# Optimization experiments

Measured on AMD Instinct MI355X. Metric: run time of the kernel, lower is better.

## Reference

```python
import jax, jax.numpy as jnp
import numpy as np

B, N, E, C = 8, 4096, 1024, 512


def setup_inputs() -> dict:
    key = jax.random.key(0)
    k1, k2, k3, k4 = jax.random.split(key, 4)
    node_feats = jax.random.normal(k1, (B, N, C), dtype=jnp.float32)
    hyper_feats = jax.random.normal(k2, (B, E, C), dtype=jnp.float32)
    # torch nn.Linear params: weight [out, in], bias [out]
    Wq = jax.random.normal(k3, (C, C), dtype=jnp.float32) * (1.0 / np.sqrt(C))
    bq = jnp.zeros((C,), dtype=jnp.float32)
    Wkv = jax.random.normal(k4, (2 * C, C), dtype=jnp.float32) * (1.0 / np.sqrt(C))
    bkv = jnp.zeros((2 * C,), dtype=jnp.float32)
    return {"node_feats": node_feats, "hyper_feats": hyper_feats,
            "Wq": Wq, "bq": bq, "Wkv": Wkv, "bkv": bkv}


def reference(node_feats, hyper_feats, Wq, bq, Wkv, bkv):
    C_ = node_feats.shape[-1]
    scale = C_ ** -0.5
    Q = node_feats @ Wq.T + bq                      # [B,N,C]
    KV = hyper_feats @ Wkv.T + bkv                  # [B,E,2C]
    K, V = KV[..., :C_], KV[..., C_:]               # [B,E,C] each
    attn = jnp.einsum('bnc,bec->bne', Q, K) * scale  # [B,N,E]
    attn = jax.nn.softmax(attn, axis=-1)
    return jnp.einsum('bne,bec->bnc', attn, V)       # [B,N,C]
```

## Files before the change

kernel.cpp:

```cpp
#include <hip/hip_runtime.h>
#include <cstdint>
#include <cstddef>

typedef _Float16 h16;
typedef _Float16 h16x4 __attribute__((ext_vector_type(4)));
typedef _Float16 h16x8 __attribute__((ext_vector_type(8)));
typedef float fx4 __attribute__((ext_vector_type(4)));

static constexpr int B_ = 8, N_ = 4096, E_ = 1024, C_ = 512;
static constexpr float SCALE = 0.044194173824159216f;

__device__ __forceinline__ void glds16(const h16* g, h16* l) {
  __builtin_amdgcn_global_load_lds(
      (const __attribute__((address_space(1))) unsigned int*)g,
      (__attribute__((address_space(3))) unsigned int*)l, 16, 0, 0);
}

__global__ __launch_bounds__(256) void cvt_kernel(const float* __restrict__ src,
                                                  h16* __restrict__ dst, int n8) {
  int i = blockIdx.x * 256 + threadIdx.x;
  if (i >= n8) return;
  const float4* s4 = (const float4*)src;
  float4 a = s4[2 * i], b = s4[2 * i + 1];
  h16x8 o;
  o[0] = (h16)a.x; o[1] = (h16)a.y; o[2] = (h16)a.z; o[3] = (h16)a.w;
  o[4] = (h16)b.x; o[5] = (h16)b.y; o[6] = (h16)b.z; o[7] = (h16)b.w;
  *(h16x8*)(dst + (size_t)i * 8) = o;
}

template <int MODE>
__global__ __launch_bounds__(256) void gemm_bt(
    const void* __restrict__ Ap, const h16* __restrict__ Bm,
    const float* __restrict__ bias,
    h16* __restrict__ outH, h16* __restrict__ outK, h16* __restrict__ outVt,
    float* __restrict__ outF, float* __restrict__ rowsum,
    int Ncols, int K) {
  constexpr bool CVT = (MODE <= 1);
  __shared__ h16 sA[128 * 32];
  __shared__ h16 sB[128 * 32];
  const int tid = threadIdx.x;
  const int wave = tid >> 6, lane = tid & 63;
  const int wm = wave >> 1, wn = wave & 1;
  const int lr = lane & 15, kq = lane >> 4;
  const int mBase = blockIdx.x * 128, nBase = blockIdx.y * 128;
  const int z = blockIdx.z;
  const h16* Ah = (const h16*)Ap;
  const float* Af = (const float*)Ap;
  if (MODE == 2) { Ah += (size_t)z * N_ * C_; Bm += (size_t)z * E_ * C_;
                   outH += (size_t)z * N_ * E_; rowsum += (size_t)z * N_; }
  if (MODE == 3) { Ah += (size_t)z * N_ * E_; Bm += (size_t)z * C_ * E_;
                   outF += (size_t)z * N_ * C_; rowsum += (size_t)z * N_; }

  fx4 acc[4][4];
#pragma unroll
  for (int i = 0; i < 4; i++)
#pragma unroll
    for (int j = 0; j < 4; j++) acc[i][j] = (fx4){0.f, 0.f, 0.f, 0.f};

  const int rowInA = lane >> 2, colInA = (lane & 3) * 8;
  const int cvtRow = tid >> 3;
  const int cvtCol = (tid & 7) * 4;

  for (int kb = 0; kb < K; kb += 32) {
    __syncthreads();
    if (CVT) {
#pragma unroll
      for (int j = 0; j < 4; j++) {
        int row = j * 32 + cvtRow;
        float4 f = *(const float4*)(Af + (size_t)(mBase + row) * K + kb + cvtCol);
        h16x4 p;
        p[0] = (h16)f.x; p[1] = (h16)f.y; p[2] = (h16)f.z; p[3] = (h16)f.w;
        *(h16x4*)&sA[row * 32 + cvtCol] = p;
      }
    } else {
#pragma unroll
      for (int i = 0; i < 2; i++) {
        int chunk = wave + i * 4;
        glds16(Ah + (size_t)(mBase + chunk * 16 + rowInA) * K + kb + colInA,
               &sA[chunk * 512]);
      }
    }
#pragma unroll
    for (int i = 0; i < 2; i++) {
      int chunk = wave + i * 4;
      glds16(Bm + (size_t)(nBase + chunk * 16 + rowInA) * K + kb + colInA,
             &sB[chunk * 512]);
    }
    __syncthreads();
    h16x8 af[4], bf[4];
#pragma unroll
    for (int mi = 0; mi < 4; mi++)
      af[mi] = *(const h16x8*)&sA[(wm * 64 + mi * 16 + lr) * 32 + kq * 8];
#pragma unroll
    for (int ni = 0; ni < 4; ni++)
      bf[ni] = *(const h16x8*)&sB[(wn * 64 + ni * 16 + lr) * 32 + kq * 8];
#pragma unroll
    for (int mi = 0; mi < 4; mi++)
#pragma unroll
      for (int ni = 0; ni < 4; ni++)
        acc[mi][ni] = __builtin_amdgcn_mfma_f32_16x16x32_f16(af[mi], bf[ni], acc[mi][ni], 0, 0, 0);
  }

  const int rb = kq * 4;
  if (MODE == 2) {
#pragma unroll
    for (int mi = 0; mi < 4; mi++) {
#pragma unroll
      for (int r = 0; r < 4; r++) {
        int row = mBase + wm * 64 + mi * 16 + rb + r;
        float rs = 0.f;
#pragma unroll
        for (int ni = 0; ni < 4; ni++) {
          int col = nBase + wn * 64 + ni * 16 + lr;
          float e = __expf(acc[mi][ni][r] * SCALE);
          rs += e;
          outH[(size_t)row * Ncols + col] = (h16)e;
        }
        rs += __shfl_xor(rs, 1); rs += __shfl_xor(rs, 2);
        rs += __shfl_xor(rs, 4); rs += __shfl_xor(rs, 8);
        if (lr == 0) atomicAdd(&rowsum[row], rs);
      }
    }
  } else if (MODE == 3) {
#pragma unroll
    for (int mi = 0; mi < 4; mi++) {
#pragma unroll
      for (int r = 0; r < 4; r++) {
        int row = mBase + wm * 64 + mi * 16 + rb + r;
        float inv = 1.0f / rowsum[row];
#pragma unroll
        for (int ni = 0; ni < 4; ni++) {
          int col = nBase + wn * 64 + ni * 16 + lr;
          outF[(size_t)row * Ncols + col] = acc[mi][ni][r] * inv;
        }
      }
    }
  } else {
#pragma unroll
    for (int mi = 0; mi < 4; mi++) {
#pragma unroll
      for (int ni = 0; ni < 4; ni++) {
        int row0 = mBase + wm * 64 + mi * 16 + rb;
        int col = nBase + wn * 64 + ni * 16 + lr;
        if (MODE == 1 && col >= C_) {
          float bv = bias[col];
          h16x4 pk;
#pragma unroll
          for (int r = 0; r < 4; r++) pk[r] = (h16)(acc[mi][ni][r] + bv);
          int zb = row0 >> 10, e = row0 & 1023;
          *(h16x4*)&outVt[((size_t)zb * C_ + (col - C_)) * E_ + e] = pk;
        } else {
#pragma unroll
          for (int r = 0; r < 4; r++) {
            int row = row0 + r;
            float v = acc[mi][ni][r] + bias[col];
            if (MODE == 0) outH[(size_t)row * Ncols + col] = (h16)v;
            else           outK[(size_t)row * C_ + col] = (h16)v;
          }
        }
      }
    }
  }
}

extern "C" void kernel_launch(void* const* d_in, const int* in_sizes, int n_in,
                              void* d_out, int out_size, void* d_ws, size_t ws_size,
                              hipStream_t stream) {
  const float* node  = (const float*)d_in[0];
  const float* hyper = (const float*)d_in[1];
  const float* Wq    = (const float*)d_in[2];
  const float* bq    = (const float*)d_in[3];
  const float* Wkv   = (const float*)d_in[4];
  const float* bkv   = (const float*)d_in[5];
  float* out = (float*)d_out;
  char* ws = (char*)d_ws;

  h16* S_h     = (h16*)(ws + 0);
  h16* Q_h     = (h16*)(ws + 67108864);
  h16* K_h     = (h16*)(ws + 100663296);
  h16* Vt_h    = (h16*)(ws + 109051904);
  h16* Wq_h    = (h16*)(ws + 117440512);
  h16* Wkv_h   = (h16*)(ws + 117964800);
  float* rowsum = (float*)(ws + 119013376);
  if (ws_size < 119144448u) return;

  cvt_kernel<<<dim3((C_ * C_ / 8 + 255) / 256), 256, 0, stream>>>(Wq, Wq_h, C_ * C_ / 8);
  cvt_kernel<<<dim3((2 * C_ * C_ / 8 + 255) / 256), 256, 0, stream>>>(Wkv, Wkv_h, 2 * C_ * C_ / 8);
  hipMemsetAsync(rowsum, 0, (size_t)B_ * N_ * sizeof(float), stream);

  gemm_bt<0><<<dim3(B_ * N_ / 128, C_ / 128), 256, 0, stream>>>(
      node, Wq_h, bq, Q_h, nullptr, nullptr, nullptr, nullptr, C_, C_);
  gemm_bt<1><<<dim3(B_ * E_ / 128, 2 * C_ / 128), 256, 0, stream>>>(
      hyper, Wkv_h, bkv, nullptr, K_h, Vt_h, nullptr, nullptr, 2 * C_, C_);
  gemm_bt<2><<<dim3(N_ / 128, E_ / 128, B_), 256, 0, stream>>>(
      Q_h, K_h, nullptr, S_h, nullptr, nullptr, nullptr, rowsum, E_, C_);
  gemm_bt<3><<<dim3(N_ / 128, C_ / 128, B_), 256, 0, stream>>>(
      S_h, Vt_h, nullptr, nullptr, nullptr, nullptr, out, rowsum, C_, E_);
}
```

Measured before the change: 309.2 us.

## Switch GEMMs to 256x256 tiles with multi-stage async LDS pipeline

Replaces the 128x128 single-buffered GEMM with a 256x256-tile, 8-wave kernel that keeps four K-stages in flight in 128KB of dynamic LDS, using swizzled layouts and explicit waitcnt/barrier scheduling with setprio around MFMA bursts. Input fp32 activations are now converted to fp16 in separate passes so every GEMM can use direct global-to-LDS loads. The aim is to hide memory latency and raise reuse per loaded byte, at the cost of extra conversion traffic, fewer blocks (lower occupancy, possible tail effects on small grids), and more fragile hand-scheduled synchronization.

```diff
diff --git a/kernel.cpp b/kernel.cpp
--- a/kernel.cpp
+++ b/kernel.cpp
@@ -29,88 +29,133 @@
 }
 
 template <int MODE>
-__global__ __launch_bounds__(256) void gemm_bt(
-    const void* __restrict__ Ap, const h16* __restrict__ Bm,
+__global__ __launch_bounds__(512) void gemm256(
+    const h16* __restrict__ A, const h16* __restrict__ Bm,
     const float* __restrict__ bias,
     h16* __restrict__ outH, h16* __restrict__ outK, h16* __restrict__ outVt,
     float* __restrict__ outF, float* __restrict__ rowsum,
     int Ncols, int K) {
-  constexpr bool CVT = (MODE <= 1);
-  __shared__ h16 sA[128 * 32];
-  __shared__ h16 sB[128 * 32];
+  extern __shared__ h16 lds[];
   const int tid = threadIdx.x;
   const int wave = tid >> 6, lane = tid & 63;
-  const int wm = wave >> 1, wn = wave & 1;
+  const int wm = wave >> 2, wn = wave & 3;
   const int lr = lane & 15, kq = lane >> 4;
-  const int mBase = blockIdx.x * 128, nBase = blockIdx.y * 128;
+  const int mBase = blockIdx.x * 256, nBase = blockIdx.y * 256;
   const int z = blockIdx.z;
-  const h16* Ah = (const h16*)Ap;
-  const float* Af = (const float*)Ap;
-  if (MODE == 2) { Ah += (size_t)z * N_ * C_; Bm += (size_t)z * E_ * C_;
+  if (MODE == 2) { A += (size_t)z * N_ * C_; Bm += (size_t)z * E_ * C_;
                    outH += (size_t)z * N_ * E_; rowsum += (size_t)z * N_; }
-  if (MODE == 3) { Ah += (size_t)z * N_ * E_; Bm += (size_t)z * C_ * E_;
+  if (MODE == 3) { A += (size_t)z * N_ * E_; Bm += (size_t)z * C_ * E_;
                    outF += (size_t)z * N_ * C_; rowsum += (size_t)z * N_; }
 
-  fx4 acc[4][4];
-#pragma unroll
-  for (int i = 0; i < 4; i++)
-#pragma unroll
-    for (int j = 0; j < 4; j++) acc[i][j] = (fx4){0.f, 0.f, 0.f, 0.f};
-
-  const int rowInA = lane >> 2, colInA = (lane & 3) * 8;
-  const int cvtRow = tid >> 3;
-  const int cvtCol = (tid & 7) * 4;
-
-  for (int kb = 0; kb < K; kb += 32) {
-    __syncthreads();
-    if (CVT) {
-#pragma unroll
-      for (int j = 0; j < 4; j++) {
-        int row = j * 32 + cvtRow;
-        float4 f = *(const float4*)(Af + (size_t)(mBase + row) * K + kb + cvtCol);
-        h16x4 p;
-        p[0] = (h16)f.x; p[1] = (h16)f.y; p[2] = (h16)f.z; p[3] = (h16)f.w;
-        *(h16x4*)&sA[row * 32 + cvtCol] = p;
-      }
+  fx4 acc[8][4];
+#pragma unroll
+  for (int i = 0; i < 8; ++i)
+#pragma unroll
+    for (int j = 0; j < 4; ++j) acc[i][j] = (fx4){0.f, 0.f, 0.f, 0.f};
+
+  float bv[4] = {0.f, 0.f, 0.f, 0.f};
+  if constexpr (MODE <= 1) {
+#pragma unroll
+    for (int ni = 0; ni < 4; ++ni) bv[ni] = bias[nBase + wn * 64 + ni * 16 + lr];
+  }
+
+  int aoff[8], boff[4];
+#pragma unroll
+  for (int f = 0; f < 8; ++f) {
+    int row = wm * 128 + f * 16 + lr;
+    int r2 = row >> 1;
+    int s8 = (((row & 1) << 2) | kq) ^ (r2 & 7);
+    aoff[f] = r2 * 64 + s8 * 8;
+  }
+#pragma unroll
+  for (int n = 0; n < 4; ++n) {
+    int row = wn * 64 + n * 16 + lr;
+    int r2 = row >> 1;
+    int s8 = (((row & 1) << 2) | kq) ^ (r2 & 7);
+    boff[n] = 8192 + r2 * 64 + s8 * 8;
+  }
+
+  size_t aSrc[2], bSrc[2];
+#pragma unroll
+  for (int i = 0; i < 2; ++i) {
+    int r2 = i * 64 + (tid >> 3);
+    int so8 = (tid & 7) ^ (r2 & 7);
+    int grow = 2 * r2 + (so8 >> 2);
+    int gcol = (so8 & 3) * 8;
+    aSrc[i] = (size_t)(mBase + grow) * K + gcol;
+    bSrc[i] = (size_t)(nBase + grow) * K + gcol;
+  }
+  const int KH = K >> 5, SU = KH * 2;
+
+  auto stage = [&](int s) {
+    int kh2 = s >> 1;
+    h16* lb = lds + (kh2 & 3) * 16384 + (s & 1) * 8192 + wave * 512;
+    int kc = kh2 * 32;
+    if ((s & 1) == 0) {
+      glds16(A + aSrc[0] + kc, lb);
+      glds16(A + aSrc[1] + kc, lb + 4096);
     } else {
-#pragma unroll
-      for (int i = 0; i < 2; i++) {
-        int chunk = wave + i * 4;
-        glds16(Ah + (size_t)(mBase + chunk * 16 + rowInA) * K + kb + colInA,
-               &sA[chunk * 512]);
-      }
-    }
-#pragma unroll
-    for (int i = 0; i < 2; i++) {
-      int chunk = wave + i * 4;
-      glds16(Bm + (size_t)(nBase + chunk * 16 + rowInA) * K + kb + colInA,
-             &sB[chunk * 512]);
-    }
-    __syncthreads();
+      glds16(Bm + bSrc[0] + kc, lb);
+      glds16(Bm + bSrc[1] + kc, lb + 4096);
+    }
+  };
+
+#pragma unroll
+  for (int s = 0; s < 5; ++s) stage(s);
+  asm volatile("s_waitcnt vmcnt(6)" ::: "memory");
+  __builtin_amdgcn_s_barrier();
+
+  int s_next = 5;
+  for (int kh = 0; kh < KH; ++kh) {
+    const int sb = (kh & 3) * 16384;
     h16x8 af[4], bf[4];
 #pragma unroll
-    for (int mi = 0; mi < 4; mi++)
-      af[mi] = *(const h16x8*)&sA[(wm * 64 + mi * 16 + lr) * 32 + kq * 8];
-#pragma unroll
-    for (int ni = 0; ni < 4; ni++)
-      bf[ni] = *(const h16x8*)&sB[(wn * 64 + ni * 16 + lr) * 32 + kq * 8];
-#pragma unroll
-    for (int mi = 0; mi < 4; mi++)
-#pragma unroll
-      for (int ni = 0; ni < 4; ni++)
-        acc[mi][ni] = __builtin_amdgcn_mfma_f32_16x16x32_f16(af[mi], bf[ni], acc[mi][ni], 0, 0, 0);
-  }
-
-  const int rb = kq * 4;
+    for (int i = 0; i < 4; ++i) af[i] = *(const h16x8*)&lds[sb + aoff[i]];
+#pragma unroll
+    for (int i = 0; i < 4; ++i) bf[i] = *(const h16x8*)&lds[sb + boff[i]];
+    if (s_next < SU) stage(s_next);
+    ++s_next;
+    __builtin_amdgcn_s_barrier();
+    asm volatile("s_waitcnt lgkmcnt(0)" ::: "memory");
+    __builtin_amdgcn_sched_barrier(0);
+    __builtin_amdgcn_s_setprio(1);
+#pragma unroll
+    for (int mi = 0; mi < 4; ++mi)
+#pragma unroll
+      for (int ni = 0; ni < 4; ++ni)
+        acc[mi][ni] = __builtin_amdgcn_mfma_f32_16x16x32_f16(af[mi], bf[ni],
+                                                             acc[mi][ni], 0, 0, 0);
+    __builtin_amdgcn_s_setprio(0);
+    __builtin_amdgcn_s_barrier();
+#pragma unroll
+    for (int i = 0; i < 4; ++i) af[i] = *(const h16x8*)&lds[sb + aoff[4 + i]];
+    if (s_next < SU) stage(s_next);
+    ++s_next;
+    asm volatile("s_waitcnt vmcnt(6)" ::: "memory");
+    __builtin_amdgcn_s_barrier();
+    asm volatile("s_waitcnt lgkmcnt(0)" ::: "memory");
+    __builtin_amdgcn_sched_barrier(0);
+    __builtin_amdgcn_s_setprio(1);
+#pragma unroll
+    for (int mi = 0; mi < 4; ++mi)
+#pragma unroll
+      for (int ni = 0; ni < 4; ++ni)
+        acc[4 + mi][ni] = __builtin_amdgcn_mfma_f32_16x16x32_f16(af[mi], bf[ni],
+                                                                 acc[4 + mi][ni], 0, 0, 0);
+    __builtin_amdgcn_s_setprio(0);
+    __builtin_amdgcn_s_barrier();
+  }
+
+  const int rbase = kq * 4;
   if (MODE == 2) {
 #pragma unroll
-    for (int mi = 0; mi < 4; mi++) {
-#pragma unroll
-      for (int r = 0; r < 4; r++) {
-        int row = mBase + wm * 64 + mi * 16 + rb + r;
+    for (int mi = 0; mi < 8; ++mi) {
+#pragma unroll
+      for (int r = 0; r < 4; ++r) {
+        int row = mBase + wm * 128 + mi * 16 + rbase + r;
         float rs = 0.f;
 #pragma unroll
-        for (int ni = 0; ni < 4; ni++) {
+        for (int ni = 0; ni < 4; ++ni) {
           int col = nBase + wn * 64 + ni * 16 + lr;
           float e = __expf(acc[mi][ni][r] * SCALE);
           rs += e;
@@ -123,13 +168,13 @@
     }
   } else if (MODE == 3) {
 #pragma unroll
-    for (int mi = 0; mi < 4; mi++) {
-#pragma unroll
-      for (int r = 0; r < 4; r++) {
-        int row = mBase + wm * 64 + mi * 16 + rb + r;
+    for (int mi = 0; mi < 8; ++mi) {
+#pragma unroll
+      for (int r = 0; r < 4; ++r) {
+        int row = mBase + wm * 128 + mi * 16 + rbase + r;
         float inv = 1.0f / rowsum[row];
 #pragma unroll
-        for (int ni = 0; ni < 4; ni++) {
+        for (int ni = 0; ni < 4; ++ni) {
           int col = nBase + wn * 64 + ni * 16 + lr;
           outF[(size_t)row * Ncols + col] = acc[mi][ni][r] * inv;
         }
@@ -137,25 +182,23 @@
     }
   } else {
 #pragma unroll
-    for (int mi = 0; mi < 4; mi++) {
-#pragma unroll
-      for (int ni = 0; ni < 4; ni++) {
-        int row0 = mBase + wm * 64 + mi * 16 + rb;
+    for (int mi = 0; mi < 8; ++mi) {
+      int row0 = mBase + wm * 128 + mi * 16 + rbase;
+#pragma unroll
+      for (int ni = 0; ni < 4; ++ni) {
         int col = nBase + wn * 64 + ni * 16 + lr;
         if (MODE == 1 && col >= C_) {
-          float bv = bias[col];
           h16x4 pk;
 #pragma unroll
-          for (int r = 0; r < 4; r++) pk[r] = (h16)(acc[mi][ni][r] + bv);
+          for (int r = 0; r < 4; ++r) pk[r] = (h16)(acc[mi][ni][r] + bv[ni]);
           int zb = row0 >> 10, e = row0 & 1023;
           *(h16x4*)&outVt[((size_t)zb * C_ + (col - C_)) * E_ + e] = pk;
         } else {
 #pragma unroll
-          for (int r = 0; r < 4; r++) {
-            int row = row0 + r;
-            float v = acc[mi][ni][r] + bias[col];
-            if (MODE == 0) outH[(size_t)row * Ncols + col] = (h16)v;
-            else           outK[(size_t)row * C_ + col] = (h16)v;
+          for (int r = 0; r < 4; ++r) {
+            float v = acc[mi][ni][r] + bv[ni];
+            if (MODE == 0) outH[(size_t)(row0 + r) * Ncols + col] = (h16)v;
+            else           outK[(size_t)(row0 + r) * C_ + col] = (h16)v;
           }
         }
       }
@@ -176,6 +219,8 @@
   char* ws = (char*)d_ws;
 
   h16* S_h     = (h16*)(ws + 0);
+  h16* node_h  = (h16*)(ws + 0);
+  h16* hyper_h = (h16*)(ws + 33554432);
   h16* Q_h     = (h16*)(ws + 67108864);
   h16* K_h     = (h16*)(ws + 100663296);
   h16* Vt_h    = (h16*)(ws + 109051904);
@@ -184,16 +229,31 @@
   float* rowsum = (float*)(ws + 119013376);
   if (ws_size < 119144448u) return;
 
-  cvt_kernel<<<dim3((C_ * C_ / 8 + 255) / 256), 256, 0, stream>>>(Wq, Wq_h, C_ * C_ / 8);
-  cvt_kernel<<<dim3((2 * C_ * C_ / 8 + 255) / 256), 256, 0, stream>>>(Wkv, Wkv_h, 2 * C_ * C_ / 8);
+  static int attr_done = 0;
+  if (!attr_done) {
+    hipFuncSetAttribute(reinterpret_cast<const void*>(&gemm256<0>),
+                        hipFuncAttributeMaxDynamicSharedMemorySize, 131072);
+    hipFuncSetAttribute(reinterpret_cast<const void*>(&gemm256<1>),
+                        hipFuncAttributeMaxDynamicSharedMemorySize, 131072);
+    hipFuncSetAttribute(reinterpret_cast<const void*>(&gemm256<2>),
+                        hipFuncAttributeMaxDynamicSharedMemorySize, 131072);
+    hipFuncSetAttribute(reinterpret_cast<const void*>(&gemm256<3>),
+                        hipFuncAttributeMaxDynamicSharedMemorySize, 131072);
+    attr_done = 1;
+  }
+
+  cvt_kernel<<<dim3(C_ * C_ / 8 / 256), 256, 0, stream>>>(Wq, Wq_h, C_ * C_ / 8);
+  cvt_kernel<<<dim3(2 * C_ * C_ / 8 / 256), 256, 0, stream>>>(Wkv, Wkv_h, 2 * C_ * C_ / 8);
+  cvt_kernel<<<dim3(B_ * N_ * C_ / 8 / 256), 256, 0, stream>>>(node, node_h, B_ * N_ * C_ / 8);
+  cvt_kernel<<<dim3(B_ * E_ * C_ / 8 / 256), 256, 0, stream>>>(hyper, hyper_h, B_ * E_ * C_ / 8);
   hipMemsetAsync(rowsum, 0, (size_t)B_ * N_ * sizeof(float), stream);
 
-  gemm_bt<0><<<dim3(B_ * N_ / 128, C_ / 128), 256, 0, stream>>>(
-      node, Wq_h, bq, Q_h, nullptr, nullptr, nullptr, nullptr, C_, C_);
-  gemm_bt<1><<<dim3(B_ * E_ / 128, 2 * C_ / 128), 256, 0, stream>>>(
-      hyper, Wkv_h, bkv, nullptr, K_h, Vt_h, nullptr, nullptr, 2 * C_, C_);
-  gemm_bt<2><<<dim3(N_ / 128, E_ / 128, B_), 256, 0, stream>>>(
+  gemm256<0><<<dim3(B_ * N_ / 256, C_ / 256), 512, 131072, stream>>>(
+      node_h, Wq_h, bq, Q_h, nullptr, nullptr, nullptr, nullptr, C_, C_);
+  gemm256<1><<<dim3(B_ * E_ / 256, 2 * C_ / 256), 512, 131072, stream>>>(
+      hyper_h, Wkv_h, bkv, nullptr, K_h, Vt_h, nullptr, nullptr, 2 * C_, C_);
+  gemm256<2><<<dim3(N_ / 256, E_ / 256, B_), 512, 131072, stream>>>(
       Q_h, K_h, nullptr, S_h, nullptr, nullptr, nullptr, rowsum, E_, C_);
-  gemm_bt<3><<<dim3(N_ / 128, C_ / 128, B_), 256, 0, stream>>>(
+  gemm256<3><<<dim3(N_ / 256, C_ / 256, B_), 512, 131072, stream>>>(
       S_h, Vt_h, nullptr, nullptr, nullptr, nullptr, out, rowsum, C_, E_);
 }
```

Measured after the change: 289.9 us. 6.3% less time.
